# Optimization experiments

Measured on AMD Instinct MI355X. Metric: run time of the kernel, lower is better.

Reference implementation:

```python
import jax, jax.numpy as jnp
import numpy as np

B, S, HID = 2, 2048, 2048
H = 16
Q_LORA = 1536
KV_LORA = 512
NOPE = 128
ROPE = 64
VDIM = 128
EPS = 1e-6
THETA = 10000.0
SCALE = 1.0 / np.sqrt(NOPE + ROPE)


def rmsnorm(x, w):
    var = jnp.mean(jnp.square(x), axis=-1, keepdims=True)
    return x * jax.lax.rsqrt(var + EPS) * w


def rotate_half(x):
    x1, x2 = jnp.split(x, 2, axis=-1)
    return jnp.concatenate([-x2, x1], axis=-1)


def setup_inputs() -> dict:
    key = jax.random.key(0)
    ks = jax.random.split(key, 10)
    w = 0.02
    hidden_states = jax.random.normal(ks[0], (B, S, HID), jnp.float32)
    # causal additive mask (bsz, 1, q_len, kv_len)
    causal = jnp.tril(jnp.ones((S, S), jnp.bool_))
    attention_mask = jnp.where(causal, 0.0, jnp.finfo(jnp.float32).min)[None, None].repeat(B, 0)
    position_ids = jnp.broadcast_to(jnp.arange(S, dtype=jnp.int64), (B, S))
    return {
        'hidden_states': hidden_states,
        'attention_mask': attention_mask,
        'q_a_w': jax.random.normal(ks[1], (Q_LORA, HID), jnp.float32) * w,
        'q_a_ln_w': jnp.ones((Q_LORA,), jnp.float32),
        'q_b_rope_w': jax.random.normal(ks[2], (H * ROPE, Q_LORA), jnp.float32) * w,
        'qk_nope_w': jax.random.normal(ks[3], (H * KV_LORA, Q_LORA), jnp.float32) * w,
        'kv_a_w': jax.random.normal(ks[4], (KV_LORA + ROPE, HID), jnp.float32) * w,
        'kv_a_ln_w': jnp.ones((KV_LORA,), jnp.float32),
        'v_b_w': jax.random.normal(ks[5], (H * VDIM, KV_LORA), jnp.float32) * w,
        'o_w': jax.random.normal(ks[6], (HID, H * VDIM), jnp.float32) * w,
        'position_ids': position_ids,
    }


def reference(hidden_states, attention_mask, q_a_w, q_a_ln_w, q_b_rope_w, qk_nope_w,
              kv_a_w, kv_a_ln_w, v_b_w, o_w, position_ids):
    b, s, _ = hidden_states.shape
    # low-rank Q path
    q_a = rmsnorm(hidden_states @ q_a_w.T, q_a_ln_w)                 # (b,s,Q_LORA)
    q_rope = (q_a @ q_b_rope_w.T).reshape(b, s, H, ROPE).transpose(0, 2, 1, 3)  # (b,h,s,rd)
    # compressed KV + shared rope key
    ckv_full = hidden_states @ kv_a_w.T                              # (b,s,KV_LORA+ROPE)
    ckv = rmsnorm(ckv_full[..., :KV_LORA], kv_a_ln_w)                # (b,s,KV_LORA)
    k_rope = ckv_full[..., KV_LORA:]                                 # (b,s,rd)
    # rotary embedding
    inv_freq = 1.0 / (THETA ** (jnp.arange(0, ROPE, 2, dtype=jnp.float32) / ROPE))
    t = jnp.arange(s, dtype=jnp.float32)
    freqs = jnp.outer(t, inv_freq)                                   # (s, rd/2)
    emb = jnp.concatenate([freqs, freqs], axis=-1)                   # (s, rd)
    cos = jnp.cos(emb)[position_ids][:, None]                        # (b,1,s,rd)
    sin = jnp.sin(emb)[position_ids][:, None]
    q_rope = q_rope * cos + rotate_half(q_rope) * sin                # (b,h,s,rd)
    k_rope = k_rope[:, None] * cos + rotate_half(k_rope[:, None]) * sin  # (b,1,s,rd)
    # absorbed nope score: q_a -> (b,h,s,KV_LORA) then vs compressed kv
    nope_q = (q_a @ qk_nope_w.T).reshape(b, s, H, KV_LORA).transpose(0, 2, 1, 3)
    nope_score = jnp.einsum('bhqc,bkc->bhqk', nope_q, ckv)
    rope_score = jnp.einsum('bhqr,bkr->bhqk', q_rope, k_rope[:, 0])
    attn = (nope_score + rope_score) * SCALE + attention_mask
    attn = jax.nn.softmax(attn.astype(jnp.float32), axis=-1).astype(hidden_states.dtype)
    # AV in compressed space, then absorbed v projection
    ctx = jnp.einsum('bhqk,bkc->bhqc', attn, ckv)                    # (b,h,q,KV_LORA)
    v_w = v_b_w.reshape(H, VDIM, KV_LORA)
    out = jnp.einsum('bhqc,hvc->bhqv', ctx, v_w)                     # (b,h,q,VDIM)
    out = out.transpose(0, 2, 1, 3).reshape(b, s, H * VDIM)
    return out @ o_w.T
```

## Files before the change

kernel.cpp:

```cpp
#include <hip/hip_runtime.h>
#include <hip/hip_bf16.h>

typedef __bf16 bf16;
typedef __bf16 bf16x8 __attribute__((ext_vector_type(8)));
typedef float f32x4 __attribute__((ext_vector_type(4)));
typedef float f32x16 __attribute__((ext_vector_type(16)));

#define AS3(p) ((__attribute__((address_space(3))) void*)(p))
#define AS1(p) ((const __attribute__((address_space(1))) void*)(p))
#define GLDS16(g,l) __builtin_amdgcn_global_load_lds(AS1(g), AS3(l), 16, 0, 0)
#define MFMA_BF16(a,b,c) __builtin_amdgcn_mfma_f32_16x16x32_bf16((a),(b),(c),0,0,0)
#define MFMA32(a,b,c) __builtin_amdgcn_mfma_f32_32x32x16_bf16((a),(b),(c),0,0,0)

constexpr int S_ = 2048;
constexpr int H_ = 16;
constexpr int KVL_ = 512;
constexpr int ROPE_ = 64;
constexpr int VD_ = 128;
constexpr int DQK_ = 576;
constexpr float SCALE_ = 0.07216878364870323f;

__device__ __forceinline__ bf16 to_bf16(float f) {
    unsigned u = __builtin_bit_cast(unsigned, f);
    unsigned r = u + 0x7FFFu + ((u >> 16) & 1u);
    unsigned short h = (unsigned short)(r >> 16);
    return __builtin_bit_cast(bf16, h);
}

__device__ __forceinline__ unsigned cvt_pk_bf16(float lo, float hi) {
    unsigned r;
    asm("v_cvt_pk_bf16_f32 %0, %1, %2" : "=v"(r) : "v"(lo), "v"(hi));
    return r;
}

__global__ void cast_kernel(const float* __restrict__ in, bf16* __restrict__ out, long n, long pad) {
    long i = ((long)blockIdx.x * 256 + threadIdx.x) * 4;
    long stride = (long)gridDim.x * 256 * 4;
    for (; i < pad; i += stride) {
        if (i < n) {
            float4 v = *(const float4*)(in + i);
            out[i + 0] = to_bf16(v.x);
            out[i + 1] = to_bf16(v.y);
            out[i + 2] = to_bf16(v.z);
            out[i + 3] = to_bf16(v.w);
        } else {
            out[i + 0] = to_bf16(0.f); out[i + 1] = to_bf16(0.f);
            out[i + 2] = to_bf16(0.f); out[i + 3] = to_bf16(0.f);
        }
    }
}

__global__ void rmsnorm_kernel(const float* __restrict__ in, const float* __restrict__ w,
                               bf16* __restrict__ out, int dim, int istride) {
    const int row = blockIdx.x;
    const float* x = in + (long)row * istride;
    float ss = 0.f;
    for (int i = threadIdx.x; i < dim; i += 256) { float v = x[i]; ss += v * v; }
#pragma unroll
    for (int d = 1; d < 64; d <<= 1) ss += __shfl_xor(ss, d);
    __shared__ float red[4];
    if ((threadIdx.x & 63) == 0) red[threadIdx.x >> 6] = ss;
    __syncthreads();
    float tot = red[0] + red[1] + red[2] + red[3];
    float rs = rsqrtf(tot / (float)dim + 1e-6f);
    for (int i = threadIdx.x; i < dim; i += 256)
        out[(long)row * dim + i] = to_bf16(x[i] * rs * w[i]);
}

__global__ void rope_table_kernel(float* __restrict__ cosT, float* __restrict__ sinT) {
    int idx = blockIdx.x * 256 + threadIdx.x;
    if (idx >= S_ * 32) return;
    int s = idx >> 5, j = idx & 31;
    float invf = expf(-(float)(2 * j) * (1.0f / 64.0f) * 9.210340371976184f);
    float a = (float)s * invf;
    cosT[idx] = cosf(a);
    sinT[idx] = sinf(a);
}

__global__ void rope_q_kernel(const float* __restrict__ qp, const float* __restrict__ cosT,
                              const float* __restrict__ sinT, bf16* __restrict__ out) {
    long bs = blockIdx.x;
    int s = (int)(bs & (S_ - 1));
    for (int e = threadIdx.x; e < H_ * ROPE_; e += 256) {
        int hh = e >> 6, i = e & 63;
        const float* x = qp + bs * (H_ * ROPE_) + hh * 64;
        float other = (i < 32) ? -x[i + 32] : x[i - 32];
        float c = cosT[s * 32 + (i & 31)], sn = sinT[s * 32 + (i & 31)];
        out[bs * (H_ * ROPE_) + e] = to_bf16((x[i] * c + other * sn) * SCALE_);
    }
}

__global__ void rope_k_kernel(const float* __restrict__ ckvf, const float* __restrict__ cosT,
                              const float* __restrict__ sinT, bf16* __restrict__ out) {
    long bs = blockIdx.x;
    int i = threadIdx.x;
    int s = (int)(bs & (S_ - 1));
    const float* x = ckvf + bs * DQK_ + KVL_;
    float other = (i < 32) ? -x[i + 32] : x[i - 32];
    float c = cosT[s * 32 + (i & 31)], sn = sinT[s * 32 + (i & 31)];
    out[bs * 64 + i] = to_bf16(x[i] * c + other * sn);
}

template <int MODE>
__global__ __launch_bounds__(256, 2)
void gemm_bt_kernel(const bf16* __restrict__ A, const bf16* __restrict__ Bm,
                    void* __restrict__ Cout, int M, int N, int K) {
    constexpr int BK = 32;
    __shared__ bf16 As[128 * BK];
    __shared__ bf16 Bs[128 * BK];
    const int tid = threadIdx.x;
    const int w = tid >> 6;
    const int lane = tid & 63;
    const long m0 = (long)blockIdx.x * 128;
    const long n0 = (long)blockIdx.y * 128;
    const int wm = (w >> 1) * 64, wn = (w & 1) * 64;
    const int lr = lane & 15;
    const int lk = (lane >> 4) * 8;

    const int c0 = w * 2, c1 = w * 2 + 1;
    const int srow0 = c0 * 16 + (lane >> 2);
    const int srow1 = c1 * 16 + (lane >> 2);
    const int skc = (lane & 3) * 8;
    const bf16* ga0 = A + (m0 + srow0) * (long)K + skc;
    const bf16* ga1 = A + (m0 + srow1) * (long)K + skc;
    const bf16* gb0 = Bm + (n0 + srow0) * (long)K + skc;
    const bf16* gb1 = Bm + (n0 + srow1) * (long)K + skc;

    f32x4 acc[4][4] = {};
    for (int kk = 0; kk < K; kk += BK) {
        __syncthreads();
        GLDS16(ga0, &As[c0 * 512]);
        GLDS16(gb0, &Bs[c0 * 512]);
        GLDS16(ga1, &As[c1 * 512]);
        GLDS16(gb1, &Bs[c1 * 512]);
        ga0 += BK; ga1 += BK; gb0 += BK; gb1 += BK;
        __syncthreads();
        bf16x8 av[4], bv[4];
#pragma unroll
        for (int i = 0; i < 4; i++) av[i] = *(const bf16x8*)&As[(wm + i * 16 + lr) * BK + lk];
#pragma unroll
        for (int j = 0; j < 4; j++) bv[j] = *(const bf16x8*)&Bs[(wn + j * 16 + lr) * BK + lk];
#pragma unroll
        for (int i = 0; i < 4; i++)
#pragma unroll
            for (int j = 0; j < 4; j++)
                acc[i][j] = MFMA_BF16(av[i], bv[j], acc[i][j]);
    }
    const int r4 = (lane >> 4) * 4;
#pragma unroll
    for (int i = 0; i < 4; i++)
#pragma unroll
        for (int j = 0; j < 4; j++) {
            long gmb = m0 + wm + i * 16 + r4;
            long gn = n0 + wn + j * 16 + lr;
#pragma unroll
            for (int r = 0; r < 4; r++) {
                long gm = gmb + r;
                float v = acc[i][j][r];
                if (MODE == 0) {
                    if (gn < N) ((float*)Cout)[gm * N + gn] = v;
                } else if (MODE == 1) {
                    if (gn < N) ((bf16*)Cout)[gm * N + gn] = to_bf16(v * SCALE_);
                } else {
                    long idx = (gm >> 11) * (2048L * 2048) + gn * 2048 + (gm & 2047);
                    ((bf16*)Cout)[idx] = to_bf16(v);
                }
            }
        }
}

__global__ __launch_bounds__(256, 2)
void flash_kernel(const bf16* __restrict__ nopeq, const bf16* __restrict__ ropeq,
                  const bf16* __restrict__ ckv, const bf16* __restrict__ krope,
                  const bf16* __restrict__ vt, bf16* __restrict__ outa) {
    __shared__ bf16 Ks2[32 * 512];
    __shared__ bf16 Krs[32 * 64];
    __shared__ char VtsB[10240];
    __shared__ char PldsB[4][32 * 80];
    const int tid = threadIdx.x;
    const int w = tid >> 6, lane = tid & 63;
    const int l31 = lane & 31;
    const int hi = lane >> 5;
    const int kel = hi * 8;
    const int klo = hi * 16;
    const int h = blockIdx.y, b = blockIdx.z;
    const int xq = (b == 0) ? (int)blockIdx.x : (15 - (int)blockIdx.x);
    const int q0 = xq * 128;
    const long bS = (long)b * S_;
    const int qg = q0 + (l31 << 2) + w;
    const int kvoff = hi * 4;

    bf16x8 qf[36];
    {
        const bf16* np = nopeq + (bS + qg) * (long)(H_ * KVL_) + h * KVL_;
        const bf16* rp = ropeq + (bS + qg) * (long)(H_ * ROPE_) + h * ROPE_;
#pragma unroll
        for (int t = 0; t < 32; ++t) qf[t] = *(const bf16x8*)(np + t * 16 + kel);
#pragma unroll
        for (int t = 0; t < 4; ++t) qf[32 + t] = *(const bf16x8*)(rp + t * 16 + kel);
    }

    unsigned soff[12];
#pragma unroll
    for (int k = 0; k < 8; ++k) {
        int c = w + 4 * k;
        soff[k] = (unsigned)((bS + c) * 1024 + ((lane * 16) ^ ((c & 7) << 4)));
    }
    {
        int rr = w * 8 + (lane >> 3);
        soff[8] = (unsigned)((bS + rr) * 128 + (((lane & 7) * 16) ^ ((rr & 7) << 4)));
    }
#pragma unroll
    for (int k = 9; k < 12; ++k) {
        int cc = (k == 11) ? (8 + w) : (w + 4 * (k - 9));
        int byt = cc * 1024 + lane * 16;
        int v = byt / 80, col = byt - v * 80;
        soff[k] = (col < 64) ? (unsigned)((((long)(b * H_ + h) * VD_ + v) * S_ + (col >> 1)) * 2) : 0u;
    }

    f32x16 accv[4] = {};
    float m_run = -3e38f, l_run = 0.f;
    const int nkv = q0 / 32 + 4;
    const int kswz = (l31 & 7) << 4;

    for (int it = 0; it < nkv; ++it) {
        const int kv0 = it * 32;
        __syncthreads();
#pragma unroll
        for (int k = 0; k < 8; ++k) {
            GLDS16((const char*)ckv + soff[k], (char*)Ks2 + (w + 4 * k) * 1024);
            soff[k] += 32768;
        }
        GLDS16((const char*)krope + soff[8], (char*)Krs + w * 1024);
        soff[8] += 4096;
        GLDS16((const char*)vt + soff[9], VtsB + w * 1024); soff[9] += 64;
        GLDS16((const char*)vt + soff[10], VtsB + (w + 4) * 1024); soff[10] += 64;
        if (w < 2) { GLDS16((const char*)vt + soff[11], VtsB + (8 + w) * 1024); soff[11] += 64; }
        __syncthreads();

        f32x16 sc = {};
        __builtin_amdgcn_s_setprio(1);
#pragma unroll
        for (int t = 0; t < 32; ++t) {
            bf16x8 kf = *(const bf16x8*)((const char*)Ks2 + l31 * 1024 + ((t * 32 + klo) ^ kswz));
            sc = MFMA32(kf, qf[t], sc);
        }
#pragma unroll
        for (int t = 0; t < 4; ++t) {
            bf16x8 kf = *(const bf16x8*)((const char*)Krs + l31 * 128 + ((t * 32 + klo) ^ kswz));
            sc = MFMA32(kf, qf[32 + t], sc);
        }
        __builtin_amdgcn_s_setprio(0);

        float s[16];
        if (kv0 + 31 > q0 + w) {
#pragma unroll
            for (int r = 0; r < 16; ++r) {
                int kvg = kv0 + kvoff + ((r & 3) + 8 * (r >> 2));
                s[r] = (kvg > qg) ? -3e38f : sc[r];
            }
        } else {
#pragma unroll
            for (int r = 0; r < 16; ++r) s[r] = sc[r];
        }

        float m8[8];
#pragma unroll
        for (int r = 0; r < 8; ++r) m8[r] = fmaxf(s[r], s[r + 8]);
        float m4a = fmaxf(m8[0], m8[1]), m4b = fmaxf(m8[2], m8[3]);
        float m4c = fmaxf(m8[4], m8[5]), m4d = fmaxf(m8[6], m8[7]);
        float mx = fmaxf(fmaxf(m4a, m4b), fmaxf(m4c, m4d));
        mx = fmaxf(mx, __shfl_xor(mx, 32));

        float mnew = fmaxf(m_run, mx);
        float corr = __expf(m_run - mnew);
#pragma unroll
        for (int r = 0; r < 16; ++r) s[r] = __expf(s[r] - mnew);
        float r8[8];
#pragma unroll
        for (int r = 0; r < 8; ++r) r8[r] = s[r] + s[r + 8];
        float r4a = r8[0] + r8[1], r4b = r8[2] + r8[3], r4c = r8[4] + r8[5], r4d = r8[6] + r8[7];
        float rs = (r4a + r4b) + (r4c + r4d);
        rs += __shfl_xor(rs, 32);

        if (__any(mnew > m_run)) {
#pragma unroll
            for (int vg = 0; vg < 4; ++vg)
#pragma unroll
                for (int r = 0; r < 16; ++r) accv[vg][r] *= corr;
        }
        l_run = l_run * corr + rs;
        m_run = mnew;

        {
            char* prow = PldsB[w] + l31 * 80;
#pragma unroll
            for (int g = 0; g < 4; ++g) {
                uint2 pk;
                pk.x = cvt_pk_bf16(s[4 * g + 0], s[4 * g + 1]);
                pk.y = cvt_pk_bf16(s[4 * g + 2], s[4 * g + 3]);
                *(uint2*)(prow + g * 16 + 8 * hi) = pk;
            }
        }
        bf16x8 pfrag[2];
#pragma unroll
        for (int c = 0; c < 2; ++c)
            pfrag[c] = *(const bf16x8*)(PldsB[w] + l31 * 80 + c * 32 + klo);

        __builtin_amdgcn_s_setprio(1);
#pragma unroll
        for (int c = 0; c < 2; ++c) {
#pragma unroll
            for (int vg = 0; vg < 4; ++vg) {
                bf16x8 vf = *(const bf16x8*)(VtsB + (vg * 32 + l31) * 80 + c * 32 + klo);
                accv[vg] = MFMA32(vf, pfrag[c], accv[vg]);
            }
        }
        __builtin_amdgcn_s_setprio(0);
    }

    float invl = 1.f / l_run;
    bf16* orow = outa + (bS + qg) * (long)(H_ * VD_) + h * VD_;
#pragma unroll
    for (int vg = 0; vg < 4; ++vg)
#pragma unroll
        for (int rq = 0; rq < 4; ++rq) {
            int vb = vg * 32 + rq * 8 + kvoff;
            ushort4 u;
            u.x = __builtin_bit_cast(unsigned short, to_bf16(accv[vg][rq * 4 + 0] * invl));
            u.y = __builtin_bit_cast(unsigned short, to_bf16(accv[vg][rq * 4 + 1] * invl));
            u.z = __builtin_bit_cast(unsigned short, to_bf16(accv[vg][rq * 4 + 2] * invl));
            u.w = __builtin_bit_cast(unsigned short, to_bf16(accv[vg][rq * 4 + 3] * invl));
            *(ushort4*)(orow + vb) = u;
        }
}

extern "C" void kernel_launch(void* const* d_in, const int* in_sizes, int n_in,
                              void* d_out, int out_size, void* d_ws, size_t ws_size,
                              hipStream_t stream) {
    const float* hidden     = (const float*)d_in[0];
    const float* q_a_w      = (const float*)d_in[2];
    const float* q_a_ln_w   = (const float*)d_in[3];
    const float* q_b_rope_w = (const float*)d_in[4];
    const float* qk_nope_w  = (const float*)d_in[5];
    const float* kv_a_w     = (const float*)d_in[6];
    const float* kv_a_ln_w  = (const float*)d_in[7];
    const float* v_b_w      = (const float*)d_in[8];
    const float* o_w        = (const float*)d_in[9];

    char* ws = (char*)d_ws;
    size_t off = 0;
    auto alloc = [&](size_t bytes) -> void* {
        void* p = ws + off;
        off += (bytes + 255) & ~(size_t)255;
        return p;
    };
    bf16* hb     = (bf16*)alloc(4096L * 2048 * 2);
    bf16* wqa    = (bf16*)alloc(1536L * 2048 * 2);
    bf16* wqr    = (bf16*)alloc(1024L * 1536 * 2);
    bf16* wnp    = (bf16*)alloc(8192L * 1536 * 2);
    bf16* wkv    = (bf16*)alloc(640L * 2048 * 2);
    bf16* wvb    = (bf16*)alloc(2048L * 512 * 2);
    bf16* wo     = (bf16*)alloc(2048L * 2048 * 2);
    float* f32scr = (float*)alloc(4096L * 1536 * 4);
    bf16* qab    = (bf16*)alloc(4096L * 1536 * 2);
    bf16* qrb    = (bf16*)alloc(4096L * 1024 * 2);
    bf16* npq    = (bf16*)alloc(4096L * 8192 * 2);
    bf16* ckvb   = (bf16*)alloc(4096L * 512 * 2);
    bf16* krb    = (bf16*)alloc(4096L * 64 * 2);
    bf16* vtb    = (bf16*)alloc(2L * 2048 * 2048 * 2);
    bf16* aout   = (bf16*)alloc(4096L * 2048 * 2);
    float* cosT  = (float*)alloc(2048L * 32 * 4);
    float* sinT  = (float*)alloc(2048L * 32 * 4);
    (void)ws_size; (void)in_sizes; (void)n_in; (void)out_size;

    cast_kernel<<<1024, 256, 0, stream>>>(hidden, hb, 8388608L, 8388608L);
    cast_kernel<<<512, 256, 0, stream>>>(q_a_w, wqa, 3145728L, 3145728L);
    cast_kernel<<<256, 256, 0, stream>>>(q_b_rope_w, wqr, 1572864L, 1572864L);
    cast_kernel<<<1024, 256, 0, stream>>>(qk_nope_w, wnp, 12582912L, 12582912L);
    cast_kernel<<<256, 256, 0, stream>>>(kv_a_w, wkv, 1179648L, 1310720L);
    cast_kernel<<<128, 256, 0, stream>>>(v_b_w, wvb, 1048576L, 1048576L);
    cast_kernel<<<512, 256, 0, stream>>>(o_w, wo, 4194304L, 4194304L);
    rope_table_kernel<<<256, 256, 0, stream>>>(cosT, sinT);

    gemm_bt_kernel<0><<<dim3(32, 12), 256, 0, stream>>>(hb, wqa, f32scr, 4096, 1536, 2048);
    rmsnorm_kernel<<<4096, 256, 0, stream>>>(f32scr, q_a_ln_w, qab, 1536, 1536);
    gemm_bt_kernel<0><<<dim3(32, 8), 256, 0, stream>>>(qab, wqr, f32scr, 4096, 1024, 1536);
    rope_q_kernel<<<4096, 256, 0, stream>>>(f32scr, cosT, sinT, qrb);
    gemm_bt_kernel<1><<<dim3(32, 64), 256, 0, stream>>>(qab, wnp, npq, 4096, 8192, 1536);
    gemm_bt_kernel<0><<<dim3(32, 5), 256, 0, stream>>>(hb, wkv, f32scr, 4096, 576, 2048);
    rmsnorm_kernel<<<4096, 256, 0, stream>>>(f32scr, kv_a_ln_w, ckvb, 512, 576);
    rope_k_kernel<<<4096, 64, 0, stream>>>(f32scr, cosT, sinT, krb);
    gemm_bt_kernel<2><<<dim3(32, 16), 256, 0, stream>>>(ckvb, wvb, vtb, 4096, 2048, 512);
    flash_kernel<<<dim3(16, 16, 2), 256, 0, stream>>>(npq, qrb, ckvb, krb, vtb, aout);
    gemm_bt_kernel<0><<<dim3(32, 16), 256, 0, stream>>>(aout, wo, (float*)d_out, 4096, 2048, 2048);
}
```

Measured before the change: 616.7 us.

## Prefetch next KV tile into LDS during softmax and PV of current tile

The attention loop now issues the global-to-LDS loads for the next KV tile right after the QK MFMAs, once the V fragments for the current tile have been read into registers and a barrier has been passed. Memory latency for the next tile can then overlap with the softmax and PV MFMA work, rather than waiting at the top of every iteration. LDS is still single-buffered. Holding the V fragments in registers costs about 32 more VGPRs per lane, which could reduce occupancy.

```diff
diff --git a/kernel.cpp b/kernel.cpp
--- a/kernel.cpp
+++ b/kernel.cpp
@@ -218,25 +218,29 @@
         soff[k] = (col < 64) ? (unsigned)((((long)(b * H_ + h) * VD_ + v) * S_ + (col >> 1)) * 2) : 0u;
     }
 
+#define STAGE() do { \
+    _Pragma("unroll") \
+    for (int k = 0; k < 8; ++k) { \
+        GLDS16((const char*)ckv + soff[k], (char*)Ks2 + (w + 4 * k) * 1024); \
+        soff[k] += 32768; \
+    } \
+    GLDS16((const char*)krope + soff[8], (char*)Krs + w * 1024); \
+    soff[8] += 4096; \
+    GLDS16((const char*)vt + soff[9], VtsB + w * 1024); soff[9] += 64; \
+    GLDS16((const char*)vt + soff[10], VtsB + (w + 4) * 1024); soff[10] += 64; \
+    if (w < 2) { GLDS16((const char*)vt + soff[11], VtsB + (8 + w) * 1024); soff[11] += 64; } \
+} while (0)
+
     f32x16 accv[4] = {};
     float m_run = -3e38f, l_run = 0.f;
     const int nkv = q0 / 32 + 4;
     const int kswz = (l31 & 7) << 4;
 
+    STAGE();
+    __syncthreads();
+
     for (int it = 0; it < nkv; ++it) {
         const int kv0 = it * 32;
-        __syncthreads();
-#pragma unroll
-        for (int k = 0; k < 8; ++k) {
-            GLDS16((const char*)ckv + soff[k], (char*)Ks2 + (w + 4 * k) * 1024);
-            soff[k] += 32768;
-        }
-        GLDS16((const char*)krope + soff[8], (char*)Krs + w * 1024);
-        soff[8] += 4096;
-        GLDS16((const char*)vt + soff[9], VtsB + w * 1024); soff[9] += 64;
-        GLDS16((const char*)vt + soff[10], VtsB + (w + 4) * 1024); soff[10] += 64;
-        if (w < 2) { GLDS16((const char*)vt + soff[11], VtsB + (8 + w) * 1024); soff[11] += 64; }
-        __syncthreads();
 
         f32x16 sc = {};
         __builtin_amdgcn_s_setprio(1);
@@ -251,6 +255,18 @@
             sc = MFMA32(kf, qf[32 + t], sc);
         }
         __builtin_amdgcn_s_setprio(0);
+
+        bf16x8 vf[8];
+#pragma unroll
+        for (int c = 0; c < 2; ++c)
+#pragma unroll
+            for (int vg = 0; vg < 4; ++vg)
+                vf[c * 4 + vg] = *(const bf16x8*)(VtsB + (vg * 32 + l31) * 80 + c * 32 + klo);
+
+        __syncthreads();
+
+        const bool has_next = (it + 1 < nkv);
+        if (has_next) STAGE();
 
         float s[16];
         if (kv0 + 31 > q0 + w) {
@@ -311,13 +327,14 @@
 #pragma unroll
         for (int c = 0; c < 2; ++c) {
 #pragma unroll
-            for (int vg = 0; vg < 4; ++vg) {
-                bf16x8 vf = *(const bf16x8*)(VtsB + (vg * 32 + l31) * 80 + c * 32 + klo);
-                accv[vg] = MFMA32(vf, pfrag[c], accv[vg]);
-            }
+            for (int vg = 0; vg < 4; ++vg)
+                accv[vg] = MFMA32(vf[c * 4 + vg], pfrag[c], accv[vg]);
         }
         __builtin_amdgcn_s_setprio(0);
-    }
+
+        if (has_next) __syncthreads();
+    }
+#undef STAGE
 
     float invl = 1.f / l_run;
     bf16* orow = outa + (bS + qg) * (long)(H_ * VD_) + h * VD_;
```

After: 767.8 us. 1.24x slower.
